# Performance work log

Measured on AMD Instinct MI355X. Metric: run time of the kernel, lower is better.

Reference implementation:

```python
import jax, jax.numpy as jnp
import numpy as np

WIN = 8          # current_window
PRETRAIN = 8     # pretrain_window
HEADS = 8
SHIFT = WIN // 2 # shift_size, shift_dir = [1, 1] (shift_mode=1)
L = WIN * WIN
LOG100 = float(np.log(100.0))


def _shift_mask(H, W):
    # bands (shift_dir=[1,1], no padding). Pairs from different regions get -100.
    hr = np.repeat(np.arange(3), [H - WIN, WIN - SHIFT, SHIFT])
    wr = np.repeat(np.arange(3), [W - WIN, WIN - SHIFT, SHIFT])
    region = hr[:, None] * 3 + wr[None, :]                      # [H, W]
    reg = region.reshape(H // WIN, WIN, W // WIN, WIN)
    reg = reg.transpose(0, 2, 1, 3).reshape(-1, L)              # [nw, L]
    m = np.where(reg[:, :, None] != reg[:, None, :], -100.0, 0.0)
    return jnp.asarray(m, dtype=jnp.float32)[None, :, None]     # [1, nw, 1, L, L]


def _rel_bias(cpb_w1, cpb_b1, cpb_w2):
    # Swin-v2 continuous relative position bias (log-spaced coords + MLP).
    pos = np.stack(np.meshgrid(np.arange(WIN), np.arange(WIN), indexing='ij'), -1).reshape(L, 2)
    rc = (pos[:, None, :] - pos[None, :, :]).astype(np.float32)  # [L, L, 2]
    rc = rc / (PRETRAIN - 1) * 8.0
    rc = np.sign(rc) * np.log2(np.abs(rc) + 1.0) / np.log2(8.0)
    rc = jnp.asarray(rc)
    bias = jax.nn.relu(rc @ cpb_w1 + cpb_b1) @ cpb_w2            # [L, L, heads]
    bias = 16.0 * jax.nn.sigmoid(bias)
    return bias.transpose(2, 0, 1)                               # [heads, L, L]


def _l2n(a):
    # tf.math.l2_normalize with epsilon=1.55e-5
    return a * jax.lax.rsqrt(jnp.maximum(jnp.sum(a * a, -1, keepdims=True), 1.55e-5))


def setup_inputs() -> dict:
    key = jax.random.key(0)
    ks = jax.random.split(key, 6)
    B, H, W, C = 16, 128, 128, 256
    cpb = 512
    return {
        'x': jax.random.normal(ks[0], (B, H, W, C), jnp.float32),
        'qkv_w': jax.random.normal(ks[1], (C, 3 * C), jnp.float32) * 0.02,
        'q_bias': jnp.zeros((C,), jnp.float32),
        'v_bias': jnp.zeros((C,), jnp.float32),
        'scale': jnp.full((HEADS, 1, 1), np.log(10.0), jnp.float32),
        'cpb_w1': jax.random.normal(ks[2], (2, cpb), jnp.float32) * 0.02,
        'cpb_b1': jnp.zeros((cpb,), jnp.float32),
        'cpb_w2': jax.random.normal(ks[3], (cpb, HEADS), jnp.float32) * 0.02,
        'proj_w': jax.random.normal(ks[4], (C, C), jnp.float32) * 0.02,
        'proj_b': jnp.zeros((C,), jnp.float32),
    }


def reference(x, qkv_w, q_bias, v_bias, scale, cpb_w1, cpb_b1, cpb_w2, proj_w, proj_b):
    B, H, W, C = x.shape
    units = C // HEADS
    # qkv 1x1 conv + (q, 0, v) bias
    bias = jnp.concatenate([q_bias, jnp.zeros_like(q_bias), v_bias])
    qkv = jnp.einsum('bhwc,cd->bhwd', x, qkv_w) + bias
    # cyclic shift (H, W > window so shift is applied; no padding needed)
    qkv = jnp.roll(qkv, (-SHIFT, -SHIFT), axis=(1, 2))
    # fused window partition -> [B, nw, heads, L, 3*units]
    nh, nw = H // WIN, W // WIN
    t = qkv.reshape(B, nh, WIN, nw, WIN, HEADS, 3 * units)
    t = t.transpose(0, 1, 3, 5, 2, 4, 6).reshape(B, nh * nw, HEADS, L, 3 * units)
    q, k, v = jnp.split(t, 3, axis=-1)
    # cosine attention with clamped learned logit scale
    logit_scale = jnp.exp(jnp.minimum(scale, LOG100))            # [heads, 1, 1]
    attn = jnp.einsum('bnhld,bnhmd->bnhlm', _l2n(q) * logit_scale, _l2n(k))
    attn = attn + _rel_bias(cpb_w1, cpb_b1, cpb_w2)[None, None] + _shift_mask(H, W)
    attn = jax.nn.softmax(attn, axis=-1)
    out = jnp.einsum('bnhlm,bnhmd->bnhld', attn, v)
    # reverse partition, reverse shift, output projection
    out = out.reshape(B, nh, nw, HEADS, WIN, WIN, units)
    out = out.transpose(0, 1, 4, 2, 5, 3, 6).reshape(B, H, W, C)
    out = jnp.roll(out, (SHIFT, SHIFT), axis=(1, 2))
    return jnp.einsum('bhwc,cd->bhwd', out, proj_w) + proj_b
```

## Files before the change

### kernel.cpp

```cpp
#include <hip/hip_runtime.h>

typedef __attribute__((ext_vector_type(4))) float  f32x4;
typedef __attribute__((ext_vector_type(8))) __bf16 bf16x8;
typedef __attribute__((ext_vector_type(4))) __bf16 bf16x4;

__global__ __launch_bounds__(256) void prep_kernel(
    const float* __restrict__ qw, const float* __restrict__ pw,
    const float* __restrict__ qb, const float* __restrict__ vb,
    const float* __restrict__ w1, const float* __restrict__ b1,
    const float* __restrict__ w2,
    __bf16* __restrict__ W2, __bf16* __restrict__ Wp,
    float* __restrict__ bcat, float* __restrict__ cpbias)
{
  if (blockIdx.x < 131) {
    int i = blockIdx.x * 256 + threadIdx.x;
    if (i < 24576) {
      int h = i / 3072, rem = i - h * 3072;
      int ft = rem >> 9, rem2 = rem & 511;
      int ks = rem2 >> 6, l = rem2 & 63;
      int g = l >> 4, c = l & 15;
      int col = h * 96 + ft * 16 + c;
      bf16x8 v;
      #pragma unroll
      for (int j = 0; j < 8; ++j)
        v[j] = (__bf16)qw[(ks * 32 + g * 8 + j) * 768 + col];
      *(bf16x8*)(W2 + (size_t)i * 8) = v;
    } else if (i < 24576 + 8192) {
      int j = i - 24576;
      int wv = j >> 10, rem = j & 1023;
      int ft = rem >> 9, rem2 = rem & 511;
      int ks = rem2 >> 6, l = rem2 & 63;
      int g = l >> 4, c = l & 15;
      int col = wv * 32 + ft * 16 + c;
      bf16x8 v;
      #pragma unroll
      for (int j8 = 0; j8 < 8; ++j8)
        v[j8] = (__bf16)pw[(ks * 32 + g * 8 + j8) * 256 + col];
      *(bf16x8*)(Wp + (size_t)j * 8) = v;
    } else if (i < 24576 + 8192 + 768) {
      int cdx = i - 24576 - 8192;
      bcat[cdx] = (cdx < 256) ? qb[cdx] : ((cdx < 512) ? 0.0f : vb[cdx - 512]);
    }
  } else {
    int pair = (blockIdx.x - 131) * 256 + threadIdx.x;
    int lq = pair >> 6, mk = pair & 63;
    float d0 = (float)((lq >> 3) - (mk >> 3));
    float d1 = (float)((lq & 7) - (mk & 7));
    float v0 = d0 * (8.0f / 7.0f);
    float v1 = d1 * (8.0f / 7.0f);
    float s0 = (v0 > 0.f) ? 1.f : ((v0 < 0.f) ? -1.f : 0.f);
    float s1 = (v1 > 0.f) ? 1.f : ((v1 < 0.f) ? -1.f : 0.f);
    float r0 = s0 * log2f(fabsf(v0) + 1.0f) * (1.0f / 3.0f);
    float r1 = s1 * log2f(fabsf(v1) + 1.0f) * (1.0f / 3.0f);
    float acc[8] = {0.f, 0.f, 0.f, 0.f, 0.f, 0.f, 0.f, 0.f};
    #pragma unroll 4
    for (int j = 0; j < 512; ++j) {
      float h = fmaxf(r0 * w1[j] + r1 * w1[512 + j] + b1[j], 0.0f);
      #pragma unroll
      for (int q = 0; q < 8; ++q) acc[q] += h * w2[j * 8 + q];
    }
    #pragma unroll
    for (int q = 0; q < 8; ++q) {
      float s = 16.0f / (1.0f + __expf(-acc[q]));
      cpbias[(q * 64 + lq) * 64 + mk] = s;
    }
  }
}

__device__ __forceinline__ int win_region(int tok, int wi, int wj) {
  int r = tok >> 3, cc = tok & 7;
  int rh = (wi == 15) ? ((r < 4) ? 1 : 2) : 0;
  int rw = (wj == 15) ? ((cc < 4) ? 1 : 2) : 0;
  return rh * 3 + rw;
}

__global__ __launch_bounds__(512, 2) void fused_kernel(
    const float* __restrict__ x, const __bf16* __restrict__ W2,
    const float* __restrict__ bcat, const float* __restrict__ scale,
    const float* __restrict__ cpb, __bf16* __restrict__ out)
{
  __shared__ __align__(16) __bf16 xs[64 * 256];
  __shared__ __align__(16) __bf16 qkp[8][64 * 72];
  __shared__ __align__(16) __bf16 vst[8][64 * 36];
  const f32x4 zz = {0.f, 0.f, 0.f, 0.f};

  int t = threadIdx.x;
  int h = t >> 6, l = t & 63, g = l >> 4, c = l & 15;
  int win = blockIdx.x, b = blockIdx.y;
  int wi = win >> 4, wj = win & 15;
  bool edge = (wi == 15) || (wj == 15);

  {
    int r = t >> 3;
    int q8 = t & 7;
    int ht = (wi * 8 + (r >> 3) + 4) & 127;
    int wt = (wj * 8 + (r & 7) + 4) & 127;
    const float* src = x + (size_t)((b * 128 + ht) * 128 + wt) * 256 + q8 * 32;
    #pragma unroll
    for (int q = 0; q < 4; ++q) {
      f32x4 a0 = *(const f32x4*)(src + q * 8);
      f32x4 a1 = *(const f32x4*)(src + q * 8 + 4);
      bf16x8 v;
      #pragma unroll
      for (int j = 0; j < 4; ++j) { v[j] = (__bf16)a0[j]; v[4 + j] = (__bf16)a1[j]; }
      int phys = (q8 * 4 + q) ^ (r & 7);
      *(bf16x8*)&xs[r * 256 + phys * 8] = v;
    }
  }
  __syncthreads();

  int toko[4];
  #pragma unroll
  for (int i = 0; i < 4; ++i) {
    int tok = 16 * i + c;
    int ht = (wi * 8 + (tok >> 3) + 4) & 127;
    int wt = (wj * 8 + (tok & 7) + 4) & 127;
    toko[i] = ((b * 128 + ht) * 128 + wt) * 256;
  }

  f32x4 acc[6][4];
  #pragma unroll
  for (int ft = 0; ft < 6; ++ft)
    #pragma unroll
    for (int tt = 0; tt < 4; ++tt) acc[ft][tt] = zz;

  const __bf16* Wh = W2 + (size_t)h * 24576;
  #pragma unroll
  for (int ks = 0; ks < 8; ++ks) {
    bf16x8 wf[6], xf[4];
    #pragma unroll
    for (int ft = 0; ft < 6; ++ft)
      wf[ft] = *(const bf16x8*)(Wh + (size_t)((ft * 8 + ks) * 64 + l) * 8);
    #pragma unroll
    for (int tt = 0; tt < 4; ++tt) {
      int phys = (ks * 4 + g) ^ (c & 7);
      xf[tt] = *(const bf16x8*)&xs[(tt * 16 + c) * 256 + phys * 8];
    }
    #pragma unroll
    for (int ft = 0; ft < 6; ++ft)
      #pragma unroll
      for (int tt = 0; tt < 4; ++tt)
        acc[ft][tt] = __builtin_amdgcn_mfma_f32_16x16x32_bf16(wf[ft], xf[tt], acc[ft][tt], 0, 0, 0);
  }

  #pragma unroll
  for (int ft = 0; ft < 6; ++ft) {
    f32x4 bb = *(const f32x4*)&bcat[h * 96 + ft * 16 + 4 * g];
    #pragma unroll
    for (int tt = 0; tt < 4; ++tt) acc[ft][tt] += bb;
  }

  float ls = __expf(fminf(scale[h], 4.6051701859880914f));

  #pragma unroll
  for (int tt = 0; tt < 4; ++tt) {
    float sq = 0.f, sk = 0.f;
    #pragma unroll
    for (int i = 0; i < 4; ++i) {
      sq += acc[0][tt][i] * acc[0][tt][i] + acc[1][tt][i] * acc[1][tt][i];
      sk += acc[2][tt][i] * acc[2][tt][i] + acc[3][tt][i] * acc[3][tt][i];
    }
    sq += __shfl_xor(sq, 16); sq += __shfl_xor(sq, 32);
    sk += __shfl_xor(sk, 16); sk += __shfl_xor(sk, 32);
    float rq = rsqrtf(fmaxf(sq, 1.55e-5f)) * ls;
    float rk = rsqrtf(fmaxf(sk, 1.55e-5f));
    __bf16* row = &qkp[h][(tt * 16 + c) * 72];
    bf16x4 w0, w1, w2, w3, v0, v1;
    #pragma unroll
    for (int i = 0; i < 4; ++i) {
      w0[i] = (__bf16)(acc[0][tt][i] * rq);
      w1[i] = (__bf16)(acc[1][tt][i] * rq);
      w2[i] = (__bf16)(acc[2][tt][i] * rk);
      w3[i] = (__bf16)(acc[3][tt][i] * rk);
      v0[i] = (__bf16)acc[4][tt][i];
      v1[i] = (__bf16)acc[5][tt][i];
    }
    *(bf16x4*)&row[4 * g]      = w0;
    *(bf16x4*)&row[16 + 4 * g] = w1;
    *(bf16x4*)&row[32 + 4 * g] = w2;
    *(bf16x4*)&row[48 + 4 * g] = w3;
    __bf16* vrow = &vst[h][(tt * 16 + c) * 36];
    *(bf16x4*)&vrow[4 * g]      = v0;
    *(bf16x4*)&vrow[16 + 4 * g] = v1;
  }

  bf16x8 kf[4], qf[4];
  #pragma unroll
  for (int i = 0; i < 4; ++i) {
    kf[i] = *(const bf16x8*)&qkp[h][(16 * i + c) * 72 + 32 + 8 * g];
    qf[i] = *(const bf16x8*)&qkp[h][(16 * i + c) * 72 + 8 * g];
  }

  float rsum[4];
  __bf16* Pw = &qkp[h][0];
  #pragma unroll
  for (int nt = 0; nt < 4; ++nt) {
    f32x4 tt4[4];
    #pragma unroll
    for (int mt = 0; mt < 4; ++mt)
      tt4[mt] = __builtin_amdgcn_mfma_f32_16x16x32_bf16(kf[mt], qf[nt], zz, 0, 0, 0);
    int q = nt * 16 + c;
    float p[16];
    #pragma unroll
    for (int mt = 0; mt < 4; ++mt) {
      f32x4 bb = *(const f32x4*)&cpb[(h * 64 + q) * 64 + mt * 16 + 4 * g];
      #pragma unroll
      for (int i = 0; i < 4; ++i) p[mt * 4 + i] = tt4[mt][i] + bb[i];
    }
    if (edge) {
      int regq = win_region(q, wi, wj);
      #pragma unroll
      for (int mt = 0; mt < 4; ++mt)
        #pragma unroll
        for (int i = 0; i < 4; ++i) {
          int k = mt * 16 + 4 * g + i;
          if (win_region(k, wi, wj) != regq) p[mt * 4 + i] -= 100.0f;
        }
    }
    float mx = -1e30f;
    #pragma unroll
    for (int j = 0; j < 16; ++j) mx = fmaxf(mx, p[j]);
    mx = fmaxf(mx, __shfl_xor(mx, 16));
    mx = fmaxf(mx, __shfl_xor(mx, 32));
    float sum = 0.f;
    #pragma unroll
    for (int j = 0; j < 16; ++j) { p[j] = __expf(p[j] - mx); sum += p[j]; }
    sum += __shfl_xor(sum, 16); sum += __shfl_xor(sum, 32);
    rsum[nt] = sum;
    #pragma unroll
    for (int mt = 0; mt < 4; ++mt) {
      bf16x4 px = { (__bf16)p[mt * 4 + 0], (__bf16)p[mt * 4 + 1],
                    (__bf16)p[mt * 4 + 2], (__bf16)p[mt * 4 + 3] };
      *(bf16x4*)&Pw[q * 72 + mt * 16 + 4 * g] = px;
    }
  }

  #pragma unroll
  for (int mh = 0; mh < 2; ++mh) {
    f32x4 oacc[4];
    #pragma unroll
    for (int nt = 0; nt < 4; ++nt) oacc[nt] = zz;
    #pragma unroll
    for (int ks = 0; ks < 2; ++ks) {
      bf16x8 va;
      #pragma unroll
      for (int j = 0; j < 8; ++j)
        va[j] = vst[h][(32 * ks + 8 * g + j) * 36 + 16 * mh + c];
      #pragma unroll
      for (int nt = 0; nt < 4; ++nt) {
        bf16x8 pfr = *(const bf16x8*)&Pw[(nt * 16 + c) * 72 + 32 * ks + 8 * g];
        oacc[nt] = __builtin_amdgcn_mfma_f32_16x16x32_bf16(va, pfr, oacc[nt], 0, 0, 0);
      }
    }
    #pragma unroll
    for (int nt = 0; nt < 4; ++nt) {
      float rinv = 1.0f / rsum[nt];
      bf16x4 ov = { (__bf16)(oacc[nt][0] * rinv), (__bf16)(oacc[nt][1] * rinv),
                    (__bf16)(oacc[nt][2] * rinv), (__bf16)(oacc[nt][3] * rinv) };
      *(bf16x4*)(out + toko[nt] + h * 32 + 16 * mh + 4 * g) = ov;
    }
  }
}

__global__ __launch_bounds__(512, 4) void proj2_kernel(
    const __bf16* __restrict__ A, const __bf16* __restrict__ Wp,
    const float* __restrict__ pb, float* __restrict__ outf)
{
  __shared__ __align__(16) __bf16 os[128 * 256];
  const f32x4 zz = {0.f, 0.f, 0.f, 0.f};
  int t = threadIdx.x;
  int wv = t >> 6, l = t & 63, g = l >> 4, c = l & 15;
  int mblk = blockIdx.x;

  {
    int r = t >> 2;
    int q4 = t & 3;
    const __bf16* src = A + (size_t)(mblk * 128 + r) * 256 + q4 * 64;
    #pragma unroll
    for (int q = 0; q < 8; ++q) {
      bf16x8 v = *(const bf16x8*)(src + q * 8);
      int phys = (q4 * 8 + q) ^ (r & 7);
      *(bf16x8*)&os[r * 256 + phys * 8] = v;
    }
  }
  __syncthreads();

  f32x4 acc[2][8];
  #pragma unroll
  for (int ft = 0; ft < 2; ++ft)
    #pragma unroll
    for (int tt = 0; tt < 8; ++tt) acc[ft][tt] = zz;

  const __bf16* Wph = Wp + (size_t)wv * 8192;
  #pragma unroll
  for (int ks = 0; ks < 8; ++ks) {
    bf16x8 w0 = *(const bf16x8*)(Wph + (size_t)((0 * 8 + ks) * 64 + l) * 8);
    bf16x8 w1 = *(const bf16x8*)(Wph + (size_t)((1 * 8 + ks) * 64 + l) * 8);
    #pragma unroll
    for (int tt = 0; tt < 8; ++tt) {
      int phys = (ks * 4 + g) ^ (c & 7);
      bf16x8 xf = *(const bf16x8*)&os[(tt * 16 + c) * 256 + phys * 8];
      acc[0][tt] = __builtin_amdgcn_mfma_f32_16x16x32_bf16(w0, xf, acc[0][tt], 0, 0, 0);
      acc[1][tt] = __builtin_amdgcn_mfma_f32_16x16x32_bf16(w1, xf, acc[1][tt], 0, 0, 0);
    }
  }

  #pragma unroll
  for (int ft = 0; ft < 2; ++ft) {
    f32x4 bb = *(const f32x4*)&pb[wv * 32 + ft * 16 + 4 * g];
    #pragma unroll
    for (int tt = 0; tt < 8; ++tt) {
      f32x4 res = acc[ft][tt] + bb;
      *(f32x4*)&outf[(size_t)(mblk * 128 + tt * 16 + c) * 256 + wv * 32 + ft * 16 + 4 * g] = res;
    }
  }
}

extern "C" void kernel_launch(void* const* d_in, const int* in_sizes, int n_in,
                              void* d_out, int out_size, void* d_ws, size_t ws_size,
                              hipStream_t stream)
{
  const float* x      = (const float*)d_in[0];
  const float* qkv_w  = (const float*)d_in[1];
  const float* q_bias = (const float*)d_in[2];
  const float* v_bias = (const float*)d_in[3];
  const float* scale  = (const float*)d_in[4];
  const float* cpb_w1 = (const float*)d_in[5];
  const float* cpb_b1 = (const float*)d_in[6];
  const float* cpb_w2 = (const float*)d_in[7];
  const float* proj_w = (const float*)d_in[8];
  const float* proj_b = (const float*)d_in[9];

  char* ws = (char*)d_ws;
  __bf16* aout = (__bf16*)(ws);
  __bf16* W2   = (__bf16*)(ws + 134217728LL);
  __bf16* Wp   = (__bf16*)(ws + 134610944LL);
  float*  bcat = (float*) (ws + 134742016LL);
  float*  cpb  = (float*) (ws + 134745088LL);

  prep_kernel<<<147, 256, 0, stream>>>(qkv_w, proj_w, q_bias, v_bias,
                                       cpb_w1, cpb_b1, cpb_w2, W2, Wp, bcat, cpb);
  fused_kernel<<<dim3(256, 16), 512, 0, stream>>>(x, W2, bcat, scale, cpb, aout);
  proj2_kernel<<<2048, 512, 0, stream>>>(aout, Wp, proj_b, (float*)d_out);
}
```

Before: 399.9 us.

## Raise wave priority around MFMA blocks and stage projection output through LDS

Wraps the MFMA loops in the fused attention kernel with s_setprio so waves issuing matrix ops are favoured over waves doing loads and softmax. Separately, the projection kernel now writes its fp32 results into a padded LDS buffer in two halves and then copies contiguous row chunks to global memory. The old path scattered 16-byte stores per lane across rows. This aims for better-coalesced output writes, at the cost of extra syncthreads and an LDS round trip that reuses the input tile buffer.

```diff
diff --git a/kernel.cpp b/kernel.cpp
--- a/kernel.cpp
+++ b/kernel.cpp
@@ -136,11 +136,13 @@
       int phys = (ks * 4 + g) ^ (c & 7);
       xf[tt] = *(const bf16x8*)&xs[(tt * 16 + c) * 256 + phys * 8];
     }
+    __builtin_amdgcn_s_setprio(1);
     #pragma unroll
     for (int ft = 0; ft < 6; ++ft)
       #pragma unroll
       for (int tt = 0; tt < 4; ++tt)
         acc[ft][tt] = __builtin_amdgcn_mfma_f32_16x16x32_bf16(wf[ft], xf[tt], acc[ft][tt], 0, 0, 0);
+    __builtin_amdgcn_s_setprio(0);
   }
 
   #pragma unroll
@@ -196,9 +198,11 @@
   #pragma unroll
   for (int nt = 0; nt < 4; ++nt) {
     f32x4 tt4[4];
+    __builtin_amdgcn_s_setprio(1);
     #pragma unroll
     for (int mt = 0; mt < 4; ++mt)
       tt4[mt] = __builtin_amdgcn_mfma_f32_16x16x32_bf16(kf[mt], qf[nt], zz, 0, 0, 0);
+    __builtin_amdgcn_s_setprio(0);
     int q = nt * 16 + c;
     float p[16];
     #pragma unroll
@@ -246,11 +250,13 @@
       #pragma unroll
       for (int j = 0; j < 8; ++j)
         va[j] = vst[h][(32 * ks + 8 * g + j) * 36 + 16 * mh + c];
+      __builtin_amdgcn_s_setprio(1);
       #pragma unroll
       for (int nt = 0; nt < 4; ++nt) {
         bf16x8 pfr = *(const bf16x8*)&Pw[(nt * 16 + c) * 72 + 32 * ks + 8 * g];
         oacc[nt] = __builtin_amdgcn_mfma_f32_16x16x32_bf16(va, pfr, oacc[nt], 0, 0, 0);
       }
+      __builtin_amdgcn_s_setprio(0);
     }
     #pragma unroll
     for (int nt = 0; nt < 4; ++nt) {
@@ -266,7 +272,9 @@
     const __bf16* __restrict__ A, const __bf16* __restrict__ Wp,
     const float* __restrict__ pb, float* __restrict__ outf)
 {
-  __shared__ __align__(16) __bf16 os[128 * 256];
+  __shared__ __align__(16) char pbuf[64 * 260 * 4];
+  __bf16* os = (__bf16*)pbuf;
+  float*  osF = (float*)pbuf;
   const f32x4 zz = {0.f, 0.f, 0.f, 0.f};
   int t = threadIdx.x;
   int wv = t >> 6, l = t & 63, g = l >> 4, c = l & 15;
@@ -305,13 +313,27 @@
     }
   }
 
-  #pragma unroll
-  for (int ft = 0; ft < 2; ++ft) {
-    f32x4 bb = *(const f32x4*)&pb[wv * 32 + ft * 16 + 4 * g];
-    #pragma unroll
-    for (int tt = 0; tt < 8; ++tt) {
-      f32x4 res = acc[ft][tt] + bb;
-      *(f32x4*)&outf[(size_t)(mblk * 128 + tt * 16 + c) * 256 + wv * 32 + ft * 16 + 4 * g] = res;
+  f32x4 bb0 = *(const f32x4*)&pb[wv * 32 + 4 * g];
+  f32x4 bb1 = *(const f32x4*)&pb[wv * 32 + 16 + 4 * g];
+
+  #pragma unroll
+  for (int half = 0; half < 2; ++half) {
+    __syncthreads();
+    #pragma unroll
+    for (int ntl = 0; ntl < 4; ++ntl) {
+      int tt = half * 4 + ntl;
+      *(f32x4*)&osF[(ntl * 16 + c) * 260 + wv * 32 + 4 * g]      = acc[0][tt] + bb0;
+      *(f32x4*)&osF[(ntl * 16 + c) * 260 + wv * 32 + 16 + 4 * g] = acc[1][tt] + bb1;
+    }
+    __syncthreads();
+    {
+      int r = t >> 3;
+      int chunk = t & 7;
+      const float* src = &osF[r * 260 + chunk * 32];
+      float* dst = &outf[(size_t)(mblk * 128 + half * 64 + r) * 256 + chunk * 32];
+      #pragma unroll
+      for (int i = 0; i < 8; ++i)
+        *(f32x4*)&dst[4 * i] = *(const f32x4*)&src[4 * i];
     }
   }
 }
```

New measurement: 437.5 us. +9.4%, slower.
